# Optimization experiments

Hardware: AMD Instinct MI355X
Metric: run time of the kernel (lower is better)

The kernel has to match this reference:

```python
import jax, jax.numpy as jnp
import numpy as np

ITERATIONS = 20  # Resonator(iterations=20)
B, F, V, D = 128, 4, 2048, 4096


def _hardsign(x):
    # bipolar normalization used by MAP-VSA multiset(normalize=True); ties -> +1
    return jnp.where(x >= 0, 1.0, -1.0).astype(x.dtype)


def setup_inputs() -> dict:
    key = jax.random.key(0)
    k1, k2 = jax.random.split(key, 2)
    # bipolar codebooks: (F, V, D)
    codebooks = _hardsign(jax.random.normal(k1, (F, V, D), dtype=jnp.float32))
    # a realistic composite input: bind (elementwise product) of one codevector per factor
    idx = jax.random.randint(k2, (B, F), 0, V)                       # (B, F)
    chosen = codebooks[jnp.arange(F)[None, :], idx]                  # (B, F, D)
    inputs = jnp.prod(chosen, axis=1)                                # (B, D)
    # standard resonator init: normalized superposition of each codebook
    init_estimates = jnp.broadcast_to(
        _hardsign(jnp.sum(codebooks, axis=1)), (B, F, D)
    ).astype(jnp.float32)                                            # (B, F, D)
    return {"inputs": inputs, "init_estimates": init_estimates, "codebooks": codebooks}


def _resonator_step(inputs, est, codebooks):
    # est: (B, F, D). rolled stack over k=1..F-1 -> (B, F, F-1, D)
    f = est.shape[-2]
    rolled = jnp.stack([jnp.roll(est, k, axis=-2) for k in range(1, f)], axis=-2)
    inv_others = jnp.prod(rolled, axis=-2)          # multibind over dim -2 -> (B, F, D)
    new_est = inputs[:, None, :] * inv_others       # bind -> (B, F, D)
    sim = jnp.einsum('bfd,fvd->bfv', new_est, codebooks)   # similarity (activation='NONE')
    # multiset(codebooks, sim, normalize=True)
    return _hardsign(jnp.einsum('bfv,fvd->bfd', sim, codebooks))


def reference(inputs, init_estimates, codebooks):
    def body(carry, i):
        est, k, done = carry
        new = _resonator_step(inputs, est, codebooks)
        eq = jnp.all(new == est)          # convergence check (fixed point)
        k = jnp.where(done, k, i)
        return (new, k, done | eq), None

    carry0 = (init_estimates, jnp.int32(0), jnp.bool_(False))
    (est, k, _), _ = jax.lax.scan(body, carry0, jnp.arange(ITERATIONS, dtype=jnp.int32))
    # cleanup: argmax of |similarity| per factor (argmax_abs=True)
    sim = jnp.einsum('bfd,fvd->bfv', est, codebooks)
    outcome = jnp.argmax(jnp.abs(sim), axis=-1)     # (B, F) int indices
    return outcome, k
```

## Files before the change

### kernel.cpp

```cpp
#include <hip/hip_runtime.h>
#include <stdint.h>

#define B_    128
#define F_    4
#define V_    2048
#define D_    4096
#define DW    64
#define VW    32
#define ITERS 20
#define NKT   16
#define NBLK  512
#define ESLOT (B_ * F_ * DW)
#define SSLOT ((size_t)F_ * B_ * V_)

typedef _Float16 half8 __attribute__((ext_vector_type(8)));
typedef float   floatx4 __attribute__((ext_vector_type(4)));

__device__ __forceinline__ void cstore64(uint64_t* p, uint64_t v) {
    __hip_atomic_store(p, v, __ATOMIC_RELAXED, __HIP_MEMORY_SCOPE_AGENT);
}
__device__ __forceinline__ void cstore32(uint32_t* p, uint32_t v) {
    __hip_atomic_store(p, v, __ATOMIC_RELAXED, __HIP_MEMORY_SCOPE_AGENT);
}

__device__ __forceinline__ void xbar(int* bar, int gen) {
    __syncthreads();
    if (threadIdx.x == 0) {
        int s = blockIdx.x & 15;
        int t = __hip_atomic_fetch_add(&bar[s * 16], 1, __ATOMIC_RELAXED,
                                       __HIP_MEMORY_SCOPE_AGENT);
        if (t == gen * (NBLK / 16) - 1)
            __hip_atomic_fetch_add(&bar[256], 1, __ATOMIC_RELAXED,
                                   __HIP_MEMORY_SCOPE_AGENT);
        int spins = 0;
        while (__hip_atomic_load(&bar[256], __ATOMIC_RELAXED,
                                 __HIP_MEMORY_SCOPE_AGENT) < gen * 16) {
            __builtin_amdgcn_s_sleep(2);
            if (++spins > (1 << 16)) break;
        }
    }
    __syncthreads();
}

__device__ __forceinline__ void pack16(const float* __restrict__ x,
                                       uint64_t* __restrict__ bits, int t) {
    const float4* p = (const float4*)x + (size_t)t * 4;
    uint32_t m = 0;
    #pragma unroll
    for (int j = 0; j < 4; ++j) {
        float4 v = p[j];
        m |= (__float_as_uint(v.x) >> 31) << (4 * j + 0);
        m |= (__float_as_uint(v.y) >> 31) << (4 * j + 1);
        m |= (__float_as_uint(v.z) >> 31) << (4 * j + 2);
        m |= (__float_as_uint(v.w) >> 31) << (4 * j + 3);
    }
    ((unsigned short*)bits)[t] = (unsigned short)m;
}

__global__ __launch_bounds__(256) void k_setup(
        const float* __restrict__ cb, const float* __restrict__ inite,
        const float* __restrict__ inputs,
        uint64_t* __restrict__ cb_bits, uint64_t* __restrict__ est0,
        uint64_t* __restrict__ in_bits,
        int* __restrict__ flags, int* __restrict__ keys) {
    int gtid = blockIdx.x * 256 + threadIdx.x;
    const int T = 512 * 256;
    const int ncb = (F_ * V_ * D_) / 16;
    for (int t = gtid; t < ncb; t += T) pack16(cb, cb_bits, t);
    pack16(inite, est0, gtid);
    if (gtid < (B_ * D_) / 16) pack16(inputs, in_bits, gtid);
    if (gtid < 32) flags[gtid] = 0;
    if (gtid < B_ * F_) keys[gtid] = 0;
}

__global__ void k_packT(const uint64_t* __restrict__ cb_bits,
                        uint64_t* __restrict__ cbT) {
    int vw = blockIdx.x, dwg = blockIdx.y, f = blockIdx.z;
    int lane = threadIdx.x & 63;
    int dw = dwg * 4 + (threadIdx.x >> 6);
    uint64_t w = cb_bits[((size_t)f * V_ + vw * 64 + lane) * DW + dw];
    uint64_t r = 0;
    for (int d2 = 0; d2 < 64; ++d2) {
        uint64_t m = __ballot((unsigned)((w >> d2) & 1));
        if (lane == d2) r = m;
    }
    cbT[((size_t)f * D_ + dw * 64 + lane) * VW + vw] = r;
}

__global__ __launch_bounds__(256, 2) void k_loop(
        const uint64_t* __restrict__ cb_bits, const uint64_t* __restrict__ cbT,
        uint64_t* __restrict__ est_base, const uint64_t* __restrict__ in_bits,
        _Float16* __restrict__ simf_base, int* __restrict__ flags, int* bar) {
    const int bid = blockIdx.x;
    const int tid = threadIdx.x;
    int g = 0;

    __shared__ __align__(16) unsigned char LDSU[65536];
    __shared__ int bd;

    const int sgrp = bid & 7;
    const int s_bt = sgrp & 3, s_fhi = sgrp >> 2;
    const int shi  = bid >> 3;
    const int s_vt = shi & 31, s_flo = shi >> 5;
    const int s_f  = s_fhi + 2 * s_flo;
    const int s_v0 = s_vt * 64, s_b0 = s_bt * 32;

    const int ggrp = bid & 7;
    const int g_mt = ggrp & 1, g_f = ggrp >> 1;
    const int g_nt = bid >> 3;
    const int g_m0 = g_mt * 64, g_n0 = g_nt * 64;

    ulonglong2* CB2 = (ulonglong2*)LDSU;
    ulonglong2* NB2 = (ulonglong2*)(LDSU + 32768);
    _Float16*   As  = (_Float16*)(LDSU + 32768);
    uint64_t*   Bb  = (uint64_t*)(LDSU + 49152);

    #pragma unroll
    for (int it = 0; it < 8; ++it) {
        int cq = it * 256 + tid;
        int r = cq >> 5, ch = cq & 31;
        const ulonglong2* src = (const ulonglong2*)(cb_bits + ((size_t)s_f * V_ + s_v0 + r) * DW);
        CB2[r * 32 + (ch ^ (r & 7))] = src[ch];
    }
    {
        const uint64_t* bsrc = cbT + ((size_t)g_f * D_ + g_n0) * VW;
        #pragma unroll
        for (int p = 0; p < 4; ++p) {
            int chunk = p * 256 + tid;
            int dloc = chunk >> 4, cw = chunk & 15;
            ulonglong2 val = *(const ulonglong2*)&bsrc[dloc * VW + cw * 2];
            *(ulonglong2*)&Bb[dloc * VW + ((cw ^ (dloc & 15)) * 2)] = val;
        }
    }

    const uint64_t SPREAD = 0x1000200040008000ull;
    const uint64_t SMASK  = 0x8000800080008000ull;
    const uint64_t PONE   = 0x3C003C003C003C00ull;

    #pragma unroll 1
    for (int i = 0; i < ITERS; ++i) {
        const uint64_t* esti = est_base + (size_t)i * ESLOT;
        uint64_t*       esto = est_base + (size_t)(i + 1) * ESLOT;
        _Float16*       simf = simf_base + (size_t)i * SSLOT;

        {
            #pragma unroll
            for (int it = 0; it < 4; ++it) {
                int cq = it * 256 + tid;
                int r = cq >> 5, ch = cq & 31;
                int b = s_b0 + r;
                const ulonglong2* iv = (const ulonglong2*)(in_bits + (size_t)b * DW);
                const uint64_t* eb = esti + (size_t)b * F_ * DW;
                ulonglong2 i2 = iv[ch];
                ulonglong2 e0 = ((const ulonglong2*)(eb + 0 * DW))[ch];
                ulonglong2 e1 = ((const ulonglong2*)(eb + 1 * DW))[ch];
                ulonglong2 e2 = ((const ulonglong2*)(eb + 2 * DW))[ch];
                ulonglong2 e3 = ((const ulonglong2*)(eb + 3 * DW))[ch];
                uint64_t ex = (s_f == 0) ? e0.x : (s_f == 1) ? e1.x : (s_f == 2) ? e2.x : e3.x;
                uint64_t ey = (s_f == 0) ? e0.y : (s_f == 1) ? e1.y : (s_f == 2) ? e2.y : e3.y;
                ulonglong2 val;
                val.x = i2.x ^ e0.x ^ e1.x ^ e2.x ^ e3.x ^ ex;
                val.y = i2.y ^ e0.y ^ e1.y ^ e2.y ^ e3.y ^ ey;
                NB2[r * 32 + (ch ^ (r & 7))] = val;
            }
            __syncthreads();

            int vv = tid & 15, bb = tid >> 4;
            int svz = vv & 7, sbz = bb & 7;
            int pc[2][4];
            #pragma unroll
            for (int j = 0; j < 2; ++j)
                #pragma unroll
                for (int ii = 0; ii < 4; ++ii) pc[j][ii] = 0;

            #pragma unroll 4
            for (int ch = 0; ch < 32; ++ch) {
                ulonglong2 c[4], n[2];
                #pragma unroll
                for (int ii = 0; ii < 4; ++ii)
                    c[ii] = CB2[(vv + 16 * ii) * 32 + (ch ^ svz)];
                #pragma unroll
                for (int j = 0; j < 2; ++j)
                    n[j] = NB2[(bb + 16 * j) * 32 + (ch ^ sbz)];
                #pragma unroll
                for (int j = 0; j < 2; ++j)
                    #pragma unroll
                    for (int ii = 0; ii < 4; ++ii)
                        pc[j][ii] += __popcll(n[j].x ^ c[ii].x) + __popcll(n[j].y ^ c[ii].y);
            }
            #pragma unroll
            for (int j = 0; j < 2; ++j) {
                int b = s_b0 + bb + 16 * j;
                #pragma unroll
                for (int ii = 0; ii < 4; ++ii) {
                    int v = s_v0 + vv + 16 * ii;
                    union { _Float16 hf; unsigned short us; } cv;
                    cv.hf = (_Float16)(2048 - pc[j][ii]);
                    int other = __shfl_xor((int)cv.us, 1, 64);
                    if (!(vv & 1)) {
                        uint32_t packv = (uint32_t)cv.us | ((uint32_t)other << 16);
                        cstore32((uint32_t*)&simf[((size_t)s_f * B_ + b) * V_ + v], packv);
                    }
                }
            }
        }
        xbar(bar, ++g);

        {
            int lane = tid & 63, wave = tid >> 6;
            int lrow = lane & 15, lq = lane >> 4;
            int wm = wave & 1, wn = wave >> 1;
            if (tid == 0) bd = 0;

            const _Float16* Ab = simf + (size_t)g_f * B_ * V_ + (size_t)g_m0 * V_;
            int arow = tid >> 4, acol = tid & 15;
            half8 areg[4];
            #pragma unroll
            for (int p = 0; p < 4; ++p)
                areg[p] = *(const half8*)&Ab[(size_t)(p * 16 + arow) * V_ + acol * 8];

            floatx4 acc[2][2] = {};

            #pragma unroll 1
            for (int kt = 0; kt < NKT; ++kt) {
                __syncthreads();
                #pragma unroll
                for (int p = 0; p < 4; ++p)
                    *(half8*)&As[(p * 16 + arow) * 128 + ((acol ^ arow) * 8)] = areg[p];
                if (kt + 1 < NKT) {
                    #pragma unroll
                    for (int p = 0; p < 4; ++p)
                        areg[p] = *(const half8*)&Ab[(size_t)(p * 16 + arow) * V_ + (kt + 1) * 128 + acol * 8];
                }
                __syncthreads();

                ulonglong2 bw[2];
                #pragma unroll
                for (int nt2 = 0; nt2 < 2; ++nt2) {
                    int dloc = wn * 32 + nt2 * 16 + lrow;
                    bw[nt2] = *(const ulonglong2*)&Bb[dloc * VW + ((kt ^ (dloc & 15)) * 2)];
                }
                #pragma unroll
                for (int ks = 0; ks < 4; ++ks) {
                    half8 af[2];
                    #pragma unroll
                    for (int mt2 = 0; mt2 < 2; ++mt2) {
                        int row = wm * 32 + mt2 * 16 + lrow;
                        af[mt2] = *(const half8*)&As[row * 128 + (((ks * 4 + lq) ^ lrow) * 8)];
                    }
                    half8 bfrag[2];
                    #pragma unroll
                    for (int nt2 = 0; nt2 < 2; ++nt2) {
                        uint64_t w = (ks < 2) ? bw[nt2].x : bw[nt2].y;
                        uint32_t byte = (uint32_t)(w >> ((((ks & 1) * 4 + lq)) * 8)) & 0xFFu;
                        union { uint64_t q[2]; half8 h; } bu;
                        bu.q[0] = (((uint64_t)(byte & 0xFu) * SPREAD) & SMASK) ^ PONE;
                        bu.q[1] = (((uint64_t)(byte >> 4)   * SPREAD) & SMASK) ^ PONE;
                        bfrag[nt2] = bu.h;
                    }
                    #pragma unroll
                    for (int mt2 = 0; mt2 < 2; ++mt2)
                        #pragma unroll
                        for (int nt2 = 0; nt2 < 2; ++nt2)
                            acc[mt2][nt2] = __builtin_amdgcn_mfma_f32_16x16x32_f16(
                                af[mt2], bfrag[nt2], acc[mt2][nt2], 0, 0, 0);
                }
            }

            __syncthreads();
            unsigned char* S = (unsigned char*)As;
            #pragma unroll
            for (int mt2 = 0; mt2 < 2; ++mt2)
                #pragma unroll
                for (int nt2 = 0; nt2 < 2; ++nt2)
                    #pragma unroll
                    for (int r = 0; r < 4; ++r) {
                        int row = wm * 32 + mt2 * 16 + lq * 4 + r;
                        int col = wn * 32 + nt2 * 16 + lrow;
                        S[row * 64 + col] = (acc[mt2][nt2][r] < 0.0f) ? 1 : 0;
                    }
            __syncthreads();
            if (tid < 64) {
                const uint64_t* Sw = (const uint64_t*)S;
                uint64_t m = 0;
                #pragma unroll
                for (int j = 0; j < 8; ++j) {
                    uint64_t w = Sw[tid * 8 + j];
                    m |= ((w * 0x0102040810204080ull) >> 56) << (8 * j);
                }
                size_t widx = ((size_t)(g_m0 + tid) * F_ + g_f) * DW + g_nt;
                uint64_t old = esti[widx];
                cstore64(&esto[widx], m);
                if (old != m) atomicOr(&bd, 1);
            }
            __syncthreads();
            if (tid == 0 && bd) atomicOr(&flags[i], 1);
        }
        if (i + 1 < ITERS) xbar(bar, ++g);
    }
}

__global__ __launch_bounds__(256) void k_argmax(
        const uint64_t* __restrict__ cb_bits,
        const uint64_t* __restrict__ est_bits,
        int* __restrict__ keys) {
    int vt = blockIdx.x, f = blockIdx.y;
    int v0 = vt * 32;
    int tid = threadIdx.x;

    __shared__ __align__(16) ulonglong2 EB2[128 * 32];
    __shared__ __align__(16) ulonglong2 CBa[32 * 32];

    #pragma unroll
    for (int it = 0; it < 16; ++it) {
        int cq = it * 256 + tid;
        int r = cq >> 5, ch = cq & 31;
        const ulonglong2* src = (const ulonglong2*)(est_bits + ((size_t)r * F_ + f) * DW);
        EB2[r * 32 + (ch ^ (r & 7))] = src[ch];
    }
    #pragma unroll
    for (int it = 0; it < 4; ++it) {
        int cq = it * 256 + tid;
        int r = cq >> 5, ch = cq & 31;
        const ulonglong2* src = (const ulonglong2*)(cb_bits + ((size_t)f * V_ + v0 + r) * DW);
        CBa[r * 32 + (ch ^ (r & 7))] = src[ch];
    }
    __syncthreads();

    int vv = tid & 15, bb = tid >> 4;
    int svz = vv & 7, sbz = bb & 7;
    int pc[8][2];
    #pragma unroll
    for (int j = 0; j < 8; ++j) { pc[j][0] = 0; pc[j][1] = 0; }

    #pragma unroll 4
    for (int ch = 0; ch < 32; ++ch) {
        ulonglong2 c[2], n[8];
        #pragma unroll
        for (int i = 0; i < 2; ++i)
            c[i] = CBa[(vv + 16 * i) * 32 + (ch ^ svz)];
        #pragma unroll
        for (int j = 0; j < 8; ++j)
            n[j] = EB2[(bb + 16 * j) * 32 + (ch ^ sbz)];
        #pragma unroll
        for (int j = 0; j < 8; ++j)
            #pragma unroll
            for (int i = 0; i < 2; ++i)
                pc[j][i] += __popcll(n[j].x ^ c[i].x) + __popcll(n[j].y ^ c[i].y);
    }

    #pragma unroll
    for (int j = 0; j < 8; ++j) {
        int kj = (int)0x80000000;
        #pragma unroll
        for (int i = 0; i < 2; ++i) {
            int v = v0 + vv + 16 * i;
            int m = 2048 - pc[j][i]; if (m < 0) m = -m;
            int key = (m << 11) | (2047 - v);
            if (key > kj) kj = key;
        }
        #pragma unroll
        for (int s = 1; s < 16; s <<= 1) {
            int o = __shfl_xor(kj, s, 64);
            if (o > kj) kj = o;
        }
        if ((tid & 15) == 0)
            atomicMax(&keys[(size_t)(bb + 16 * j) * F_ + f], kj);
    }
}

__global__ void k_final(const int* __restrict__ keys, const int* __restrict__ flags,
                        int* __restrict__ out) {
    int tid = blockIdx.x * blockDim.x + threadIdx.x;
    if (tid < B_ * F_) out[tid] = 2047 - (keys[tid] & 0x7FF);
    if (tid == 0) {
        int k = ITERS - 1;
        for (int i = 0; i < ITERS; ++i) if (flags[i] == 0) { k = i; break; }
        out[B_ * F_] = k;
    }
}

extern "C" void kernel_launch(void* const* d_in, const int* in_sizes, int n_in,
                              void* d_out, int out_size, void* d_ws, size_t ws_size,
                              hipStream_t stream) {
    const float* inputs = (const float*)d_in[0];
    const float* inite  = (const float*)d_in[1];
    const float* cb     = (const float*)d_in[2];
    int* out = (int*)d_out;

    char* ws = (char*)d_ws;
    uint64_t* cb_bits  = (uint64_t*)ws;  ws += (size_t)F_ * V_ * DW * 8;
    uint64_t* cbT_bits = (uint64_t*)ws;  ws += (size_t)F_ * D_ * VW * 8;
    uint64_t* est_base = (uint64_t*)ws;  ws += (size_t)(ITERS + 1) * ESLOT * 8;
    uint64_t* in_bits  = (uint64_t*)ws;  ws += (size_t)B_ * DW * 8;
    _Float16* simf     = (_Float16*)ws;  ws += (size_t)ITERS * SSLOT * 2;
    int*      flags    = (int*)ws;       ws += 32 * 4;
    int*      keys     = (int*)ws;       ws += B_ * F_ * 4;
    int*      bar      = (int*)ws;       ws += 2048;

    hipMemsetAsync(bar, 0, 2048, stream);

    k_setup<<<512, 256, 0, stream>>>(cb, inite, inputs, cb_bits, est_base,
                                     in_bits, flags, keys);
    k_packT<<<dim3(32, 16, 4), 256, 0, stream>>>(cb_bits, cbT_bits);
    k_loop<<<NBLK, 256, 0, stream>>>(cb_bits, cbT_bits, est_base, in_bits,
                                     simf, flags, bar);
    k_argmax<<<dim3(64, 4), 256, 0, stream>>>(cb_bits,
                                              est_base + (size_t)ITERS * ESLOT, keys);
    k_final<<<2, 256, 0, stream>>>(keys, flags, out);
}
```

Before: 902.1 us.

## Double block count with half-size tiles and per-iteration operand reloads

Doubles the persistent grid from 512 to 1024 blocks. Each block now handles half as many codevectors in the popcount similarity stage and half as many output columns (32 instead of 64) in the MFMA projection stage. LDS per block is halved and occupancy raised to 4 blocks per CU, so codebook tiles no longer fit resident and are reloaded from global memory each iteration. The aim is more parallelism and latency hiding, at the cost of extra global traffic, a grid barrier across twice as many blocks, and 32-bit rather than 64-bit estimate stores.

```diff
diff --git a/kernel.cpp b/kernel.cpp
--- a/kernel.cpp
+++ b/kernel.cpp
@@ -9,16 +9,13 @@
 #define VW    32
 #define ITERS 20
 #define NKT   16
-#define NBLK  512
+#define NBLK  1024
 #define ESLOT (B_ * F_ * DW)
 #define SSLOT ((size_t)F_ * B_ * V_)
 
 typedef _Float16 half8 __attribute__((ext_vector_type(8)));
 typedef float   floatx4 __attribute__((ext_vector_type(4)));
 
-__device__ __forceinline__ void cstore64(uint64_t* p, uint64_t v) {
-    __hip_atomic_store(p, v, __ATOMIC_RELAXED, __HIP_MEMORY_SCOPE_AGENT);
-}
 __device__ __forceinline__ void cstore32(uint32_t* p, uint32_t v) {
     __hip_atomic_store(p, v, __ATOMIC_RELAXED, __HIP_MEMORY_SCOPE_AGENT);
 }
@@ -87,7 +84,7 @@
     cbT[((size_t)f * D_ + dw * 64 + lane) * VW + vw] = r;
 }
 
-__global__ __launch_bounds__(256, 2) void k_loop(
+__global__ __launch_bounds__(256, 4) void k_loop(
         const uint64_t* __restrict__ cb_bits, const uint64_t* __restrict__ cbT,
         uint64_t* __restrict__ est_base, const uint64_t* __restrict__ in_bits,
         _Float16* __restrict__ simf_base, int* __restrict__ flags, int* bar) {
@@ -95,43 +92,13 @@
     const int tid = threadIdx.x;
     int g = 0;
 
-    __shared__ __align__(16) unsigned char LDSU[65536];
+    __shared__ __align__(16) unsigned char LDSU[32768];
     __shared__ int bd;
 
-    const int sgrp = bid & 7;
-    const int s_bt = sgrp & 3, s_fhi = sgrp >> 2;
-    const int shi  = bid >> 3;
-    const int s_vt = shi & 31, s_flo = shi >> 5;
-    const int s_f  = s_fhi + 2 * s_flo;
-    const int s_v0 = s_vt * 64, s_b0 = s_bt * 32;
-
-    const int ggrp = bid & 7;
-    const int g_mt = ggrp & 1, g_f = ggrp >> 1;
-    const int g_nt = bid >> 3;
-    const int g_m0 = g_mt * 64, g_n0 = g_nt * 64;
-
-    ulonglong2* CB2 = (ulonglong2*)LDSU;
-    ulonglong2* NB2 = (ulonglong2*)(LDSU + 32768);
-    _Float16*   As  = (_Float16*)(LDSU + 32768);
-    uint64_t*   Bb  = (uint64_t*)(LDSU + 49152);
-
-    #pragma unroll
-    for (int it = 0; it < 8; ++it) {
-        int cq = it * 256 + tid;
-        int r = cq >> 5, ch = cq & 31;
-        const ulonglong2* src = (const ulonglong2*)(cb_bits + ((size_t)s_f * V_ + s_v0 + r) * DW);
-        CB2[r * 32 + (ch ^ (r & 7))] = src[ch];
-    }
-    {
-        const uint64_t* bsrc = cbT + ((size_t)g_f * D_ + g_n0) * VW;
-        #pragma unroll
-        for (int p = 0; p < 4; ++p) {
-            int chunk = p * 256 + tid;
-            int dloc = chunk >> 4, cw = chunk & 15;
-            ulonglong2 val = *(const ulonglong2*)&bsrc[dloc * VW + cw * 2];
-            *(ulonglong2*)&Bb[dloc * VW + ((cw ^ (dloc & 15)) * 2)] = val;
-        }
-    }
+    const int s_vt = bid & 63, s_bt = (bid >> 6) & 3, s_f = bid >> 8;
+    const int s_v0 = s_vt * 32, s_b0 = s_bt * 32;
+    const int g_mt = bid & 1, g_f = (bid >> 1) & 3, g_nt = bid >> 3;
+    const int g_m0 = g_mt * 64, g_n0 = g_nt * 32;
 
     const uint64_t SPREAD = 0x1000200040008000ull;
     const uint64_t SMASK  = 0x8000800080008000ull;
@@ -144,6 +111,15 @@
         _Float16*       simf = simf_base + (size_t)i * SSLOT;
 
         {
+            ulonglong2* CB2 = (ulonglong2*)LDSU;
+            ulonglong2* NB2 = (ulonglong2*)(LDSU + 16384);
+            #pragma unroll
+            for (int it = 0; it < 4; ++it) {
+                int cq = it * 256 + tid;
+                int r = cq >> 5, ch = cq & 31;
+                const ulonglong2* src = (const ulonglong2*)(cb_bits + ((size_t)s_f * V_ + s_v0 + r) * DW);
+                CB2[r * 32 + (ch ^ (r & 7))] = src[ch];
+            }
             #pragma unroll
             for (int it = 0; it < 4; ++it) {
                 int cq = it * 256 + tid;
@@ -167,17 +143,17 @@
 
             int vv = tid & 15, bb = tid >> 4;
             int svz = vv & 7, sbz = bb & 7;
-            int pc[2][4];
+            int pc[2][2];
             #pragma unroll
             for (int j = 0; j < 2; ++j)
                 #pragma unroll
-                for (int ii = 0; ii < 4; ++ii) pc[j][ii] = 0;
+                for (int ii = 0; ii < 2; ++ii) pc[j][ii] = 0;
 
             #pragma unroll 4
             for (int ch = 0; ch < 32; ++ch) {
-                ulonglong2 c[4], n[2];
-                #pragma unroll
-                for (int ii = 0; ii < 4; ++ii)
+                ulonglong2 c[2], n[2];
+                #pragma unroll
+                for (int ii = 0; ii < 2; ++ii)
                     c[ii] = CB2[(vv + 16 * ii) * 32 + (ch ^ svz)];
                 #pragma unroll
                 for (int j = 0; j < 2; ++j)
@@ -185,14 +161,14 @@
                 #pragma unroll
                 for (int j = 0; j < 2; ++j)
                     #pragma unroll
-                    for (int ii = 0; ii < 4; ++ii)
+                    for (int ii = 0; ii < 2; ++ii)
                         pc[j][ii] += __popcll(n[j].x ^ c[ii].x) + __popcll(n[j].y ^ c[ii].y);
             }
             #pragma unroll
             for (int j = 0; j < 2; ++j) {
                 int b = s_b0 + bb + 16 * j;
                 #pragma unroll
-                for (int ii = 0; ii < 4; ++ii) {
+                for (int ii = 0; ii < 2; ++ii) {
                     int v = s_v0 + vv + 16 * ii;
                     union { _Float16 hf; unsigned short us; } cv;
                     cv.hf = (_Float16)(2048 - pc[j][ii]);
@@ -210,7 +186,19 @@
             int lane = tid & 63, wave = tid >> 6;
             int lrow = lane & 15, lq = lane >> 4;
             int wm = wave & 1, wn = wave >> 1;
+
+            _Float16* As = (_Float16*)LDSU;
+            uint64_t* Bb = (uint64_t*)(LDSU + 16384);
             if (tid == 0) bd = 0;
+
+            const uint64_t* bsrc = cbT + ((size_t)g_f * D_ + g_n0) * VW;
+            #pragma unroll
+            for (int p = 0; p < 2; ++p) {
+                int chunk = p * 256 + tid;
+                int dloc = chunk >> 4, cw = chunk & 15;
+                ulonglong2 val = *(const ulonglong2*)&bsrc[dloc * VW + cw * 2];
+                *(ulonglong2*)&Bb[dloc * VW + ((cw ^ (dloc & 15)) * 2)] = val;
+            }
 
             const _Float16* Ab = simf + (size_t)g_f * B_ * V_ + (size_t)g_m0 * V_;
             int arow = tid >> 4, acol = tid & 15;
@@ -219,7 +207,7 @@
             for (int p = 0; p < 4; ++p)
                 areg[p] = *(const half8*)&Ab[(size_t)(p * 16 + arow) * V_ + acol * 8];
 
-            floatx4 acc[2][2] = {};
+            floatx4 acc[2] = {};
 
             #pragma unroll 1
             for (int kt = 0; kt < NKT; ++kt) {
@@ -234,12 +222,8 @@
                 }
                 __syncthreads();
 
-                ulonglong2 bw[2];
-                #pragma unroll
-                for (int nt2 = 0; nt2 < 2; ++nt2) {
-                    int dloc = wn * 32 + nt2 * 16 + lrow;
-                    bw[nt2] = *(const ulonglong2*)&Bb[dloc * VW + ((kt ^ (dloc & 15)) * 2)];
-                }
+                int dloc = wn * 16 + lrow;
+                ulonglong2 bw = *(const ulonglong2*)&Bb[dloc * VW + ((kt ^ (dloc & 15)) * 2)];
                 #pragma unroll
                 for (int ks = 0; ks < 4; ++ks) {
                     half8 af[2];
@@ -248,22 +232,15 @@
                         int row = wm * 32 + mt2 * 16 + lrow;
                         af[mt2] = *(const half8*)&As[row * 128 + (((ks * 4 + lq) ^ lrow) * 8)];
                     }
-                    half8 bfrag[2];
-                    #pragma unroll
-                    for (int nt2 = 0; nt2 < 2; ++nt2) {
-                        uint64_t w = (ks < 2) ? bw[nt2].x : bw[nt2].y;
-                        uint32_t byte = (uint32_t)(w >> ((((ks & 1) * 4 + lq)) * 8)) & 0xFFu;
-                        union { uint64_t q[2]; half8 h; } bu;
-                        bu.q[0] = (((uint64_t)(byte & 0xFu) * SPREAD) & SMASK) ^ PONE;
-                        bu.q[1] = (((uint64_t)(byte >> 4)   * SPREAD) & SMASK) ^ PONE;
-                        bfrag[nt2] = bu.h;
-                    }
+                    uint64_t w = (ks < 2) ? bw.x : bw.y;
+                    uint32_t byte = (uint32_t)(w >> ((((ks & 1) * 4 + lq)) * 8)) & 0xFFu;
+                    union { uint64_t q[2]; half8 h; } bu;
+                    bu.q[0] = (((uint64_t)(byte & 0xFu) * SPREAD) & SMASK) ^ PONE;
+                    bu.q[1] = (((uint64_t)(byte >> 4)   * SPREAD) & SMASK) ^ PONE;
                     #pragma unroll
                     for (int mt2 = 0; mt2 < 2; ++mt2)
-                        #pragma unroll
-                        for (int nt2 = 0; nt2 < 2; ++nt2)
-                            acc[mt2][nt2] = __builtin_amdgcn_mfma_f32_16x16x32_f16(
-                                af[mt2], bfrag[nt2], acc[mt2][nt2], 0, 0, 0);
+                        acc[mt2] = __builtin_amdgcn_mfma_f32_16x16x32_f16(
+                            af[mt2], bu.h, acc[mt2], 0, 0, 0);
                 }
             }
 
@@ -272,25 +249,23 @@
             #pragma unroll
             for (int mt2 = 0; mt2 < 2; ++mt2)
                 #pragma unroll
-                for (int nt2 = 0; nt2 < 2; ++nt2)
-                    #pragma unroll
-                    for (int r = 0; r < 4; ++r) {
-                        int row = wm * 32 + mt2 * 16 + lq * 4 + r;
-                        int col = wn * 32 + nt2 * 16 + lrow;
-                        S[row * 64 + col] = (acc[mt2][nt2][r] < 0.0f) ? 1 : 0;
-                    }
+                for (int r = 0; r < 4; ++r) {
+                    int row = wm * 32 + mt2 * 16 + lq * 4 + r;
+                    int col = wn * 16 + lrow;
+                    S[row * 32 + col] = (acc[mt2][r] < 0.0f) ? 1 : 0;
+                }
             __syncthreads();
             if (tid < 64) {
                 const uint64_t* Sw = (const uint64_t*)S;
-                uint64_t m = 0;
-                #pragma unroll
-                for (int j = 0; j < 8; ++j) {
-                    uint64_t w = Sw[tid * 8 + j];
-                    m |= ((w * 0x0102040810204080ull) >> 56) << (8 * j);
-                }
-                size_t widx = ((size_t)(g_m0 + tid) * F_ + g_f) * DW + g_nt;
-                uint64_t old = esti[widx];
-                cstore64(&esto[widx], m);
+                uint32_t m = 0;
+                #pragma unroll
+                for (int j = 0; j < 4; ++j) {
+                    uint64_t w = Sw[tid * 4 + j];
+                    m |= (uint32_t)((w * 0x0102040810204080ull) >> 56) << (8 * j);
+                }
+                size_t widx = ((size_t)(g_m0 + tid) * F_ + g_f) * (DW * 2) + g_nt;
+                uint32_t old = ((const uint32_t*)esti)[widx];
+                cstore32((uint32_t*)esto + widx, m);
                 if (old != m) atomicOr(&bd, 1);
             }
             __syncthreads();
```

After: 995.2 us. 1.1x slower.

## Fuse setup, transpose, argmax and final into one persistent kernel

Applied to the files above, without the earlier changes.

Folds the bit-packing setup, codebook transpose, final argmax and output write into the persistent loop kernel, separating the phases with the grid barrier instead of separate launches. The barrier is made hierarchical: only eight leader blocks poll the global counter and then publish per-group release flags. The fp16 sign expansion switches from multiply/mask arithmetic to a 16-entry LDS lookup table, and packing now produces 32 bits per thread. This removes several kernel launch gaps at the cost of extra barriers, and the grid barrier still depends on all 512 blocks being co-resident.

```diff
diff --git a/kernel.cpp b/kernel.cpp
--- a/kernel.cpp
+++ b/kernel.cpp
@@ -33,70 +33,92 @@
             __hip_atomic_fetch_add(&bar[256], 1, __ATOMIC_RELAXED,
                                    __HIP_MEMORY_SCOPE_AGENT);
         int spins = 0;
-        while (__hip_atomic_load(&bar[256], __ATOMIC_RELAXED,
-                                 __HIP_MEMORY_SCOPE_AGENT) < gen * 16) {
-            __builtin_amdgcn_s_sleep(2);
-            if (++spins > (1 << 16)) break;
+        if (blockIdx.x < 8) {
+            while (__hip_atomic_load(&bar[256], __ATOMIC_RELAXED,
+                                     __HIP_MEMORY_SCOPE_AGENT) < gen * 16) {
+                __builtin_amdgcn_s_sleep(2);
+                if (++spins > (1 << 16)) break;
+            }
+            __hip_atomic_store(&bar[288 + blockIdx.x * 32], gen,
+                               __ATOMIC_RELAXED, __HIP_MEMORY_SCOPE_AGENT);
+        } else {
+            while (__hip_atomic_load(&bar[288 + (blockIdx.x & 7) * 32],
+                                     __ATOMIC_RELAXED,
+                                     __HIP_MEMORY_SCOPE_AGENT) < gen) {
+                __builtin_amdgcn_s_sleep(2);
+                if (++spins > (1 << 16)) break;
+            }
         }
     }
     __syncthreads();
 }
 
-__device__ __forceinline__ void pack16(const float* __restrict__ x,
-                                       uint64_t* __restrict__ bits, int t) {
-    const float4* p = (const float4*)x + (size_t)t * 4;
+__device__ __forceinline__ void pack32c(const float* __restrict__ x,
+                                        uint32_t* __restrict__ bits, int t) {
+    const float4* p = (const float4*)x + (size_t)t * 8;
     uint32_t m = 0;
     #pragma unroll
-    for (int j = 0; j < 4; ++j) {
+    for (int j = 0; j < 8; ++j) {
         float4 v = p[j];
         m |= (__float_as_uint(v.x) >> 31) << (4 * j + 0);
         m |= (__float_as_uint(v.y) >> 31) << (4 * j + 1);
         m |= (__float_as_uint(v.z) >> 31) << (4 * j + 2);
         m |= (__float_as_uint(v.w) >> 31) << (4 * j + 3);
     }
-    ((unsigned short*)bits)[t] = (unsigned short)m;
-}
-
-__global__ __launch_bounds__(256) void k_setup(
-        const float* __restrict__ cb, const float* __restrict__ inite,
+    cstore32(&bits[t], m);
+}
+
+__global__ __launch_bounds__(256, 2) void k_loop(
+        const float* __restrict__ cbf, const float* __restrict__ inite,
         const float* __restrict__ inputs,
-        uint64_t* __restrict__ cb_bits, uint64_t* __restrict__ est0,
-        uint64_t* __restrict__ in_bits,
-        int* __restrict__ flags, int* __restrict__ keys) {
-    int gtid = blockIdx.x * 256 + threadIdx.x;
-    const int T = 512 * 256;
-    const int ncb = (F_ * V_ * D_) / 16;
-    for (int t = gtid; t < ncb; t += T) pack16(cb, cb_bits, t);
-    pack16(inite, est0, gtid);
-    if (gtid < (B_ * D_) / 16) pack16(inputs, in_bits, gtid);
-    if (gtid < 32) flags[gtid] = 0;
-    if (gtid < B_ * F_) keys[gtid] = 0;
-}
-
-__global__ void k_packT(const uint64_t* __restrict__ cb_bits,
-                        uint64_t* __restrict__ cbT) {
-    int vw = blockIdx.x, dwg = blockIdx.y, f = blockIdx.z;
-    int lane = threadIdx.x & 63;
-    int dw = dwg * 4 + (threadIdx.x >> 6);
-    uint64_t w = cb_bits[((size_t)f * V_ + vw * 64 + lane) * DW + dw];
-    uint64_t r = 0;
-    for (int d2 = 0; d2 < 64; ++d2) {
-        uint64_t m = __ballot((unsigned)((w >> d2) & 1));
-        if (lane == d2) r = m;
-    }
-    cbT[((size_t)f * D_ + dw * 64 + lane) * VW + vw] = r;
-}
-
-__global__ __launch_bounds__(256, 2) void k_loop(
-        const uint64_t* __restrict__ cb_bits, const uint64_t* __restrict__ cbT,
-        uint64_t* __restrict__ est_base, const uint64_t* __restrict__ in_bits,
-        _Float16* __restrict__ simf_base, int* __restrict__ flags, int* bar) {
+        uint64_t* __restrict__ cb_bits, uint64_t* __restrict__ cbT,
+        uint64_t* __restrict__ est_base, uint64_t* __restrict__ in_bits,
+        _Float16* __restrict__ simf_base, int* __restrict__ flags,
+        int* __restrict__ keys, int* __restrict__ out, int* bar) {
     const int bid = blockIdx.x;
     const int tid = threadIdx.x;
+    const int gtid = bid * 256 + tid;
     int g = 0;
 
     __shared__ __align__(16) unsigned char LDSU[65536];
+    __shared__ uint64_t LUT16[16];
     __shared__ int bd;
+
+    if (tid < 16) {
+        uint64_t e = 0;
+        #pragma unroll
+        for (int j = 0; j < 4; ++j)
+            e |= (((tid >> j) & 1) ? 0xBC00ull : 0x3C00ull) << (16 * j);
+        LUT16[tid] = e;
+    }
+
+    {
+        const int ncb = (F_ * V_ * D_) / 32;
+        for (int t = gtid; t < ncb; t += NBLK * 256)
+            pack32c(cbf, (uint32_t*)cb_bits, t);
+        if (gtid < (B_ * F_ * D_) / 32) pack32c(inite, (uint32_t*)est_base, gtid);
+        if (gtid < (B_ * D_) / 32)      pack32c(inputs, (uint32_t*)in_bits, gtid);
+        if (gtid < 32)      cstore32((uint32_t*)&flags[gtid], 0);
+        if (gtid < B_ * F_) cstore32((uint32_t*)&keys[gtid], 0);
+    }
+    xbar(bar, ++g);
+
+    {
+        int wave = tid >> 6, lane = tid & 63;
+        #pragma unroll 1
+        for (int s = 0; s < 4; ++s) {
+            int u = (bid * 4 + wave) + 2048 * s;
+            int vw = u & 31, dw = (u >> 5) & 63, f = u >> 11;
+            uint64_t w = cb_bits[((size_t)f * V_ + vw * 64 + lane) * DW + dw];
+            uint64_t r = 0;
+            for (int d2 = 0; d2 < 64; ++d2) {
+                uint64_t m = __ballot((unsigned)((w >> d2) & 1));
+                if (lane == d2) r = m;
+            }
+            cstore64(&cbT[((size_t)f * D_ + dw * 64 + lane) * VW + vw], r);
+        }
+    }
+    xbar(bar, ++g);
 
     const int sgrp = bid & 7;
     const int s_bt = sgrp & 3, s_fhi = sgrp >> 2;
@@ -132,10 +154,6 @@
             *(ulonglong2*)&Bb[dloc * VW + ((cw ^ (dloc & 15)) * 2)] = val;
         }
     }
-
-    const uint64_t SPREAD = 0x1000200040008000ull;
-    const uint64_t SMASK  = 0x8000800080008000ull;
-    const uint64_t PONE   = 0x3C003C003C003C00ull;
 
     #pragma unroll 1
     for (int i = 0; i < ITERS; ++i) {
@@ -254,8 +272,8 @@
                         uint64_t w = (ks < 2) ? bw[nt2].x : bw[nt2].y;
                         uint32_t byte = (uint32_t)(w >> ((((ks & 1) * 4 + lq)) * 8)) & 0xFFu;
                         union { uint64_t q[2]; half8 h; } bu;
-                        bu.q[0] = (((uint64_t)(byte & 0xFu) * SPREAD) & SMASK) ^ PONE;
-                        bu.q[1] = (((uint64_t)(byte >> 4)   * SPREAD) & SMASK) ^ PONE;
+                        bu.q[0] = LUT16[byte & 0xFu];
+                        bu.q[1] = LUT16[byte >> 4];
                         bfrag[nt2] = bu.h;
                     }
                     #pragma unroll
@@ -296,87 +314,82 @@
             __syncthreads();
             if (tid == 0 && bd) atomicOr(&flags[i], 1);
         }
-        if (i + 1 < ITERS) xbar(bar, ++g);
-    }
-}
-
-__global__ __launch_bounds__(256) void k_argmax(
-        const uint64_t* __restrict__ cb_bits,
-        const uint64_t* __restrict__ est_bits,
-        int* __restrict__ keys) {
-    int vt = blockIdx.x, f = blockIdx.y;
-    int v0 = vt * 32;
-    int tid = threadIdx.x;
-
-    __shared__ __align__(16) ulonglong2 EB2[128 * 32];
-    __shared__ __align__(16) ulonglong2 CBa[32 * 32];
-
-    #pragma unroll
-    for (int it = 0; it < 16; ++it) {
-        int cq = it * 256 + tid;
-        int r = cq >> 5, ch = cq & 31;
-        const ulonglong2* src = (const ulonglong2*)(est_bits + ((size_t)r * F_ + f) * DW);
-        EB2[r * 32 + (ch ^ (r & 7))] = src[ch];
-    }
-    #pragma unroll
-    for (int it = 0; it < 4; ++it) {
-        int cq = it * 256 + tid;
-        int r = cq >> 5, ch = cq & 31;
-        const ulonglong2* src = (const ulonglong2*)(cb_bits + ((size_t)f * V_ + v0 + r) * DW);
-        CBa[r * 32 + (ch ^ (r & 7))] = src[ch];
-    }
-    __syncthreads();
-
-    int vv = tid & 15, bb = tid >> 4;
-    int svz = vv & 7, sbz = bb & 7;
-    int pc[8][2];
-    #pragma unroll
-    for (int j = 0; j < 8; ++j) { pc[j][0] = 0; pc[j][1] = 0; }
-
-    #pragma unroll 4
-    for (int ch = 0; ch < 32; ++ch) {
-        ulonglong2 c[2], n[8];
-        #pragma unroll
-        for (int i = 0; i < 2; ++i)
-            c[i] = CBa[(vv + 16 * i) * 32 + (ch ^ svz)];
-        #pragma unroll
-        for (int j = 0; j < 8; ++j)
-            n[j] = EB2[(bb + 16 * j) * 32 + (ch ^ sbz)];
-        #pragma unroll
-        for (int j = 0; j < 8; ++j)
-            #pragma unroll
-            for (int i = 0; i < 2; ++i)
-                pc[j][i] += __popcll(n[j].x ^ c[i].x) + __popcll(n[j].y ^ c[i].y);
-    }
-
-    #pragma unroll
-    for (int j = 0; j < 8; ++j) {
-        int kj = (int)0x80000000;
-        #pragma unroll
-        for (int i = 0; i < 2; ++i) {
-            int v = v0 + vv + 16 * i;
-            int m = 2048 - pc[j][i]; if (m < 0) m = -m;
-            int key = (m << 11) | (2047 - v);
-            if (key > kj) kj = key;
-        }
-        #pragma unroll
-        for (int s = 1; s < 16; s <<= 1) {
-            int o = __shfl_xor(kj, s, 64);
-            if (o > kj) kj = o;
-        }
-        if ((tid & 15) == 0)
-            atomicMax(&keys[(size_t)(bb + 16 * j) * F_ + f], kj);
-    }
-}
-
-__global__ void k_final(const int* __restrict__ keys, const int* __restrict__ flags,
-                        int* __restrict__ out) {
-    int tid = blockIdx.x * blockDim.x + threadIdx.x;
-    if (tid < B_ * F_) out[tid] = 2047 - (keys[tid] & 0x7FF);
-    if (tid == 0) {
-        int k = ITERS - 1;
-        for (int i = 0; i < ITERS; ++i) if (flags[i] == 0) { k = i; break; }
-        out[B_ * F_] = k;
+        xbar(bar, ++g);
+    }
+
+    {
+        const uint64_t* estF = est_base + (size_t)ITERS * ESLOT;
+        int vt = bid & 63, bg = (bid >> 6) & 1, f = bid >> 7;
+        int v0 = vt * 32, b0g = bg * 64;
+        ulonglong2* EB2 = (ulonglong2*)LDSU;
+        ulonglong2* CBa = (ulonglong2*)(LDSU + 32768);
+        #pragma unroll
+        for (int it = 0; it < 8; ++it) {
+            int cq = it * 256 + tid;
+            int r = cq >> 5, ch = cq & 31;
+            const ulonglong2* src = (const ulonglong2*)(estF + ((size_t)(b0g + r) * F_ + f) * DW);
+            EB2[r * 32 + (ch ^ (r & 7))] = src[ch];
+        }
+        #pragma unroll
+        for (int it = 0; it < 4; ++it) {
+            int cq = it * 256 + tid;
+            int r = cq >> 5, ch = cq & 31;
+            const ulonglong2* src = (const ulonglong2*)(cb_bits + ((size_t)f * V_ + v0 + r) * DW);
+            CBa[r * 32 + (ch ^ (r & 7))] = src[ch];
+        }
+        __syncthreads();
+
+        int vv = tid & 15, bb = tid >> 4;
+        int svz = vv & 7, sbz = bb & 7;
+        int pc[4][2];
+        #pragma unroll
+        for (int j = 0; j < 4; ++j) { pc[j][0] = 0; pc[j][1] = 0; }
+
+        #pragma unroll 4
+        for (int ch = 0; ch < 32; ++ch) {
+            ulonglong2 c[2], n[4];
+            #pragma unroll
+            for (int ii = 0; ii < 2; ++ii)
+                c[ii] = CBa[(vv + 16 * ii) * 32 + (ch ^ svz)];
+            #pragma unroll
+            for (int j = 0; j < 4; ++j)
+                n[j] = EB2[(bb + 16 * j) * 32 + (ch ^ sbz)];
+            #pragma unroll
+            for (int j = 0; j < 4; ++j)
+                #pragma unroll
+                for (int ii = 0; ii < 2; ++ii)
+                    pc[j][ii] += __popcll(n[j].x ^ c[ii].x) + __popcll(n[j].y ^ c[ii].y);
+        }
+        #pragma unroll
+        for (int j = 0; j < 4; ++j) {
+            int kj = (int)0x80000000;
+            #pragma unroll
+            for (int ii = 0; ii < 2; ++ii) {
+                int v = v0 + vv + 16 * ii;
+                int m = 2048 - pc[j][ii]; if (m < 0) m = -m;
+                int key = (m << 11) | (2047 - v);
+                if (key > kj) kj = key;
+            }
+            #pragma unroll
+            for (int s = 1; s < 16; s <<= 1) {
+                int o = __shfl_xor(kj, s, 64);
+                if (o > kj) kj = o;
+            }
+            if ((tid & 15) == 0)
+                atomicMax(&keys[(size_t)(b0g + bb + 16 * j) * F_ + f], kj);
+        }
+    }
+    xbar(bar, ++g);
+
+    if (bid == 0) {
+        for (int t = tid; t < B_ * F_; t += 256)
+            cstore32((uint32_t*)&out[t], (uint32_t)(2047 - (keys[t] & 0x7FF)));
+        if (tid == 0) {
+            int k = ITERS - 1;
+            for (int i2 = 0; i2 < ITERS; ++i2)
+                if (flags[i2] == 0) { k = i2; break; }
+            cstore32((uint32_t*)&out[B_ * F_], (uint32_t)k);
+        }
     }
 }
 
@@ -396,16 +409,11 @@
     _Float16* simf     = (_Float16*)ws;  ws += (size_t)ITERS * SSLOT * 2;
     int*      flags    = (int*)ws;       ws += 32 * 4;
     int*      keys     = (int*)ws;       ws += B_ * F_ * 4;
-    int*      bar      = (int*)ws;       ws += 2048;
-
-    hipMemsetAsync(bar, 0, 2048, stream);
-
-    k_setup<<<512, 256, 0, stream>>>(cb, inite, inputs, cb_bits, est_base,
-                                     in_bits, flags, keys);
-    k_packT<<<dim3(32, 16, 4), 256, 0, stream>>>(cb_bits, cbT_bits);
-    k_loop<<<NBLK, 256, 0, stream>>>(cb_bits, cbT_bits, est_base, in_bits,
-                                     simf, flags, bar);
-    k_argmax<<<dim3(64, 4), 256, 0, stream>>>(cb_bits,
-                                              est_base + (size_t)ITERS * ESLOT, keys);
-    k_final<<<2, 256, 0, stream>>>(keys, flags, out);
-}
+    int*      bar      = (int*)ws;       ws += 4096;
+
+    hipMemsetAsync(bar, 0, 4096, stream);
+
+    k_loop<<<NBLK, 256, 0, stream>>>(cb, inite, inputs, cb_bits, cbT_bits,
+                                     est_base, in_bits, simf, flags, keys,
+                                     out, bar);
+}
```

New measurement: 845.1 us. 1.07x faster.
